# Performance work log

Measured on AMD Instinct MI355X. Metric: run time of the kernel, lower is better.

The kernel has to match this reference:

```python
import jax, jax.numpy as jnp
import numpy as np

N_NODES = 50000
IN_CH = 128
OUT_CH = 64
HEADS = 2
N_EDGES = 400000
NEG_SLOPE = 0.2  # PyG GATConv default


def _glorot(key, shape):
    fan_in, fan_out = shape[0], shape[-1]
    lim = jnp.sqrt(6.0 / (fan_in + fan_out))
    return jax.random.uniform(key, shape, jnp.float32, -lim, lim)


def setup_inputs() -> dict:
    key = jax.random.key(0)
    ks = jax.random.split(key, 12)
    hid = 2 * OUT_CH  # per-head channels of conv1
    inp = {
        "x": jax.random.normal(ks[0], (N_NODES, IN_CH), jnp.float32),
        "edge_index": jax.random.randint(ks[1], (2, N_EDGES), 0, N_NODES, jnp.int32),
        # conv1: in=IN_CH, out=hid per head, HEADS heads, concat
        "W1": _glorot(ks[2], (IN_CH, HEADS * hid)),
        "att_src1": _glorot(ks[3], (HEADS, hid)),
        "att_dst1": _glorot(ks[4], (HEADS, hid)),
        "b1": jnp.zeros((HEADS * hid,), jnp.float32),
        # conv_mu: in=hid*HEADS, out=OUT_CH, 1 head
        "W_mu": _glorot(ks[5], (hid * HEADS, OUT_CH)),
        "att_src_mu": _glorot(ks[6], (1, OUT_CH)),
        "att_dst_mu": _glorot(ks[7], (1, OUT_CH)),
        "b_mu": jnp.zeros((OUT_CH,), jnp.float32),
        # conv_logstd: same shapes as conv_mu
        "W_ls": _glorot(ks[8], (hid * HEADS, OUT_CH)),
        "att_src_ls": _glorot(ks[9], (1, OUT_CH)),
        "att_dst_ls": _glorot(ks[10], (1, OUT_CH)),
        "b_ls": jnp.zeros((OUT_CH,), jnp.float32),
    }
    return inp


def gat_conv(x, src, dst, W, att_src, att_dst, b, n_nodes):
    """PyG GATConv (add_self_loops handled by caller in src/dst)."""
    H, C = att_src.shape
    h = (x @ W).reshape(n_nodes, H, C)                       # [N,H,C]
    a_src = jnp.einsum('nhc,hc->nh', h, att_src)             # [N,H]
    a_dst = jnp.einsum('nhc,hc->nh', h, att_dst)
    e = jax.nn.leaky_relu(a_src[src] + a_dst[dst], NEG_SLOPE)  # [E,H]
    # scatter-softmax over incoming edges per destination node
    m = jax.ops.segment_max(e, dst, num_segments=n_nodes)
    e = jnp.exp(e - m[dst])
    denom = jax.ops.segment_sum(e, dst, num_segments=n_nodes)
    alpha = e / (denom[dst] + 1e-16)                          # [E,H]
    out = jax.ops.segment_sum(h[src] * alpha[:, :, None], dst,
                              num_segments=n_nodes)           # [N,H,C]
    return out.reshape(n_nodes, H * C) + b


def reference(x, edge_index, W1, att_src1, att_dst1, b1,
              W_mu, att_src_mu, att_dst_mu, b_mu,
              W_ls, att_src_ls, att_dst_ls, b_ls):
    n = x.shape[0]
    loop = jnp.arange(n, dtype=edge_index.dtype)
    src = jnp.concatenate([edge_index[0], loop])  # add self-loops (PyG default)
    dst = jnp.concatenate([edge_index[1], loop])
    h = jax.nn.elu(gat_conv(x, src, dst, W1, att_src1, att_dst1, b1, n))
    mu = gat_conv(h, src, dst, W_mu, att_src_mu, att_dst_mu, b_mu, n)
    logstd = gat_conv(h, src, dst, W_ls, att_src_ls, att_dst_ls, b_ls, n)
    return (mu, logstd)
```

## Files before the change

### kernel.cpp

```cpp
#include <hip/hip_runtime.h>
#include <math.h>

#define N_NODES 50000
#define N_EDGES 400000
#define PAD 64

typedef __attribute__((ext_vector_type(8))) short bf16x8;
typedef __attribute__((ext_vector_type(4))) float f32x4;

__device__ __forceinline__ float lrelu(float x){ return x > 0.f ? x : 0.2f*x; }
__device__ __forceinline__ float bf2f(unsigned short u){ return __uint_as_float(((unsigned int)u)<<16); }
__device__ __forceinline__ unsigned short f2bf(float f){
    unsigned int b = __float_as_uint(f);
    return (unsigned short)((b + 0x7FFFu + ((b>>16)&1u)) >> 16);
}
__device__ __forceinline__ float4 bf4(ushort4 u){
    return make_float4(bf2f(u.x), bf2f(u.y), bf2f(u.z), bf2f(u.w));
}
__device__ __forceinline__ float wexp(float e){ return __expf(fminf(e, 80.f)); }

__global__ __launch_bounds__(256) void prep_k(const float* __restrict__ x, unsigned short* __restrict__ xb,
        const float* __restrict__ W1, const float* __restrict__ Wmu, const float* __restrict__ Wls,
        unsigned short* __restrict__ W1T, unsigned short* __restrict__ WmlT,
        const int* __restrict__ src, const int* __restrict__ dst,
        int* __restrict__ counts, int* __restrict__ csr_src){
    int i = blockIdx.x*256 + threadIdx.x;
    if (i < (N_NODES*128)/4){
        float4 v = ((const float4*)x)[i];
        ((ushort4*)xb)[i] = make_ushort4(f2bf(v.x), f2bf(v.y), f2bf(v.z), f2bf(v.w));
    }
    if (i < 32768){
        int n = i >> 7, k = i & 127;
        W1T[i] = f2bf(W1[k*256 + n]);
        int n2 = i >> 8, k2 = i & 255;
        float v = (n2 < 64) ? Wmu[k2*64 + n2] : Wls[k2*64 + (n2-64)];
        WmlT[i] = f2bf(v);
    }
    if (i < N_EDGES){
        int d = dst[i];
        int pos = atomicAdd(&counts[d], 1);
        csr_src[d*PAD + pos] = src[i];
    }
}

template<int MODE>
__global__ __launch_bounds__(256) void mfma_gemm_k(const unsigned short* __restrict__ A,
        const unsigned short* __restrict__ BT, unsigned short* __restrict__ C,
        int M, int K, int ldc,
        const float* __restrict__ attS0, const float* __restrict__ attD0,
        const float* __restrict__ attS1, const float* __restrict__ attD1,
        float* __restrict__ outS, float* __restrict__ outD){
    __shared__ unsigned short As[128*40];
    __shared__ unsigned short Bs[128*40];
    int t = threadIdx.x;
    int lane = t & 63, wid = t >> 6;
    int wy = wid >> 1, wx = wid & 1;
    int quad = lane >> 4, l15 = lane & 15;
    int row0 = blockIdx.y * 128;
    int col0 = blockIdx.x * 128;

    f32x4 acc[4][4];
    #pragma unroll
    for (int i = 0; i < 4; i++)
        #pragma unroll
        for (int j = 0; j < 4; j++)
            acc[i][j] = (f32x4){0.f, 0.f, 0.f, 0.f};

    int r = t >> 2;
    int cofs = (t & 3) * 8;

    for (int k0 = 0; k0 < K; k0 += 32){
        int gr0 = min(row0 + r,      M-1);
        int gr1 = min(row0 + r + 64, M-1);
        float4 av0 = *(const float4*)(A  + (size_t)gr0*K + k0 + cofs);
        float4 av1 = *(const float4*)(A  + (size_t)gr1*K + k0 + cofs);
        float4 bv0 = *(const float4*)(BT + (size_t)(col0 + r)*K      + k0 + cofs);
        float4 bv1 = *(const float4*)(BT + (size_t)(col0 + r + 64)*K + k0 + cofs);
        __syncthreads();
        *(float4*)&As[r*40 + cofs]      = av0;
        *(float4*)&As[(r+64)*40 + cofs] = av1;
        *(float4*)&Bs[r*40 + cofs]      = bv0;
        *(float4*)&Bs[(r+64)*40 + cofs] = bv1;
        __syncthreads();

        bf16x8 af[4], bf[4];
        #pragma unroll
        for (int i = 0; i < 4; i++)
            af[i] = *(const bf16x8*)&As[(wy*64 + i*16 + l15)*40 + quad*8];
        #pragma unroll
        for (int j = 0; j < 4; j++)
            bf[j] = *(const bf16x8*)&Bs[(wx*64 + j*16 + l15)*40 + quad*8];
        #pragma unroll
        for (int i = 0; i < 4; i++)
            #pragma unroll
            for (int j = 0; j < 4; j++)
                acc[i][j] = __builtin_amdgcn_mfma_f32_16x16x32_bf16(af[i], bf[j], acc[i][j], 0, 0, 0);
    }

    int head = blockIdx.x;
    float aS[4], aD[4];
    #pragma unroll
    for (int j = 0; j < 4; j++){
        if (MODE == 1){
            int ch = wx*64 + j*16 + l15;
            aS[j] = attS0[head*128 + ch];
            aD[j] = attD0[head*128 + ch];
        } else {
            int c2 = j*16 + l15;
            aS[j] = wx ? attS1[c2] : attS0[c2];
            aD[j] = wx ? attD1[c2] : attD0[c2];
        }
    }

    #pragma unroll
    for (int i = 0; i < 4; i++){
        #pragma unroll
        for (int reg = 0; reg < 4; reg++){
            int rr = row0 + wy*64 + i*16 + quad*4 + reg;
            float sp = 0.f, dp = 0.f;
            #pragma unroll
            for (int j = 0; j < 4; j++){
                float v = acc[i][j][reg];
                int cc = col0 + wx*64 + j*16 + l15;
                if (rr < M) C[(size_t)rr*ldc + cc] = f2bf(v);
                sp = fmaf(v, aS[j], sp);
                dp = fmaf(v, aD[j], dp);
            }
            #pragma unroll
            for (int msk = 1; msk < 16; msk <<= 1){
                sp += __shfl_xor(sp, msk);
                dp += __shfl_xor(dp, msk);
            }
            if (l15 == 0 && rr < M){
                if (MODE == 1){
                    atomicAdd(&outS[rr*2 + head], sp);
                    atomicAdd(&outD[rr*2 + head], dp);
                } else {
                    outS[rr*2 + wx] = sp;
                    outD[rr*2 + wx] = dp;
                }
            }
        }
    }
}

__global__ __launch_bounds__(256) void agg1_k(const unsigned short* __restrict__ h1,
        const float* __restrict__ as, const float* __restrict__ ad,
        const int* __restrict__ counts, const int* __restrict__ csr_src,
        const float* __restrict__ b1, unsigned short* __restrict__ hout){
    int wave = threadIdx.x >> 6, lane = threadIdx.x & 63;
    int n = blockIdx.x*4 + wave;
    if (n >= N_NODES) return;
    int head = lane >> 5;
    const ushort4* h1v = (const ushort4*)h1;

    float adh = ad[n*2 + head];
    float ash = as[n*2 + head];

    float w = wexp(lrelu(ash + adh));
    float l = w;
    float4 r = bf4(h1v[(size_t)n*64 + lane]);
    float4 acc = make_float4(w*r.x, w*r.y, w*r.z, w*r.w);

    int deg = counts[n];
    int off = n*PAD;
    int dm1 = deg - 1;
    for (int k = 0; k < deg; k += 8){
        int sidx[8];
        #pragma unroll
        for (int u = 0; u < 8; u++) sidx[u] = csr_src[off + min(k+u, dm1)];
        float w8[8];
        #pragma unroll
        for (int u = 0; u < 8; u++){
            float av = as[sidx[u]*2 + head];
            w8[u] = (k+u <= dm1) ? wexp(lrelu(av + adh)) : 0.f;
        }
        #pragma unroll
        for (int u = 0; u < 8; u++){
            float4 ru = bf4(h1v[(size_t)sidx[u]*64 + lane]);
            float wu = w8[u];
            l += wu;
            acc.x = fmaf(wu, ru.x, acc.x);
            acc.y = fmaf(wu, ru.y, acc.y);
            acc.z = fmaf(wu, ru.z, acc.z);
            acc.w = fmaf(wu, ru.w, acc.w);
        }
    }

    float invl = 1.f / (l + 1e-16f);
    float4 b4 = *(const float4*)&b1[lane*4];
    float4 v;
    v.x = acc.x*invl + b4.x; v.y = acc.y*invl + b4.y;
    v.z = acc.z*invl + b4.z; v.w = acc.w*invl + b4.w;
    v.x = v.x > 0.f ? v.x : __expf(v.x) - 1.f;
    v.y = v.y > 0.f ? v.y : __expf(v.y) - 1.f;
    v.z = v.z > 0.f ? v.z : __expf(v.z) - 1.f;
    v.w = v.w > 0.f ? v.w : __expf(v.w) - 1.f;
    ((ushort4*)hout)[(size_t)n*64 + lane] = make_ushort4(f2bf(v.x), f2bf(v.y), f2bf(v.z), f2bf(v.w));
}

__global__ __launch_bounds__(256) void agg2_k(const unsigned short* __restrict__ hml,
        const float* __restrict__ as, const float* __restrict__ ad,
        const int* __restrict__ counts, const int* __restrict__ csr_src,
        const float* __restrict__ b_mu, const float* __restrict__ b_ls,
        float* __restrict__ out){
    int grp = threadIdx.x >> 5, lane = threadIdx.x & 31;
    int n = blockIdx.x*8 + grp;
    if (n >= N_NODES) return;
    int g = lane >> 4;
    const ushort4* hv = (const ushort4*)hml;

    float adh = ad[n*2 + g];
    float ash = as[n*2 + g];

    float w = wexp(lrelu(ash + adh));
    float l = w;
    float4 r = bf4(hv[(size_t)n*32 + lane]);
    float4 acc = make_float4(w*r.x, w*r.y, w*r.z, w*r.w);

    int deg = counts[n];
    int off = n*PAD;
    int dm1 = deg - 1;
    for (int k = 0; k < deg; k += 8){
        int sidx[8];
        #pragma unroll
        for (int u = 0; u < 8; u++) sidx[u] = csr_src[off + min(k+u, dm1)];
        float w8[8];
        #pragma unroll
        for (int u = 0; u < 8; u++){
            float av = as[sidx[u]*2 + g];
            w8[u] = (k+u <= dm1) ? wexp(lrelu(av + adh)) : 0.f;
        }
        #pragma unroll
        for (int u = 0; u < 8; u++){
            float4 ru = bf4(hv[(size_t)sidx[u]*32 + lane]);
            float wu = w8[u];
            l += wu;
            acc.x = fmaf(wu, ru.x, acc.x);
            acc.y = fmaf(wu, ru.y, acc.y);
            acc.z = fmaf(wu, ru.z, acc.z);
            acc.w = fmaf(wu, ru.w, acc.w);
        }
    }

    float invl = 1.f / (l + 1e-16f);
    int c = (lane & 15) * 4;
    const float* bb = g ? b_ls : b_mu;
    float4 b4 = *(const float4*)&bb[c];
    float4 v;
    v.x = acc.x*invl + b4.x; v.y = acc.y*invl + b4.y;
    v.z = acc.z*invl + b4.z; v.w = acc.w*invl + b4.w;
    float* base = g ? (out + (size_t)N_NODES*64) : out;
    *(float4*)&base[(size_t)n*64 + c] = v;
}

extern "C" void kernel_launch(void* const* d_in, const int* in_sizes, int n_in,
                              void* d_out, int out_size, void* d_ws, size_t ws_size,
                              hipStream_t stream) {
    const float* x           = (const float*)d_in[0];
    const int*   ei          = (const int*)d_in[1];
    const float* W1          = (const float*)d_in[2];
    const float* att_src1    = (const float*)d_in[3];
    const float* att_dst1    = (const float*)d_in[4];
    const float* b1          = (const float*)d_in[5];
    const float* W_mu        = (const float*)d_in[6];
    const float* att_src_mu  = (const float*)d_in[7];
    const float* att_dst_mu  = (const float*)d_in[8];
    const float* b_mu        = (const float*)d_in[9];
    const float* W_ls        = (const float*)d_in[10];
    const float* att_src_ls  = (const float*)d_in[11];
    const float* att_dst_ls  = (const float*)d_in[12];
    const float* b_ls        = (const float*)d_in[13];
    float* out = (float*)d_out;

    const int* srcp = ei;
    const int* dstp = ei + N_EDGES;

    unsigned short* xb   = (unsigned short*)d_ws;
    unsigned short* h1   = xb   + (size_t)N_NODES*128;
    unsigned short* hbuf = h1   + (size_t)N_NODES*256;
    unsigned short* hml  = hbuf + (size_t)N_NODES*256;
    unsigned short* W1T  = hml  + (size_t)N_NODES*128;
    unsigned short* WmlT = W1T  + 32768;
    int*   counts = (int*)(WmlT + 32768);
    float* as1    = (float*)(counts + N_NODES);
    float* ad1    = as1 + 2*N_NODES;
    float* as2    = ad1 + 2*N_NODES;
    float* ad2    = as2 + 2*N_NODES;
    int*   csr    = (int*)(ad2 + 2*N_NODES);

    hipMemsetAsync(counts, 0, N_NODES*sizeof(int) + 4*N_NODES*sizeof(float), stream);

    prep_k<<<(N_NODES*128/4 + 255)/256, 256, 0, stream>>>(x, xb, W1, W_mu, W_ls, W1T, WmlT,
                                                          srcp, dstp, counts, csr);

    mfma_gemm_k<1><<<dim3(2, 391), 256, 0, stream>>>(xb, W1T, h1, N_NODES, 128, 256,
                                                     att_src1, att_dst1, nullptr, nullptr, as1, ad1);
    agg1_k<<<(N_NODES + 3) / 4, 256, 0, stream>>>(h1, as1, ad1, counts, csr, b1, hbuf);

    mfma_gemm_k<2><<<dim3(1, 391), 256, 0, stream>>>(hbuf, WmlT, hml, N_NODES, 256, 128,
                                                     att_src_mu, att_dst_mu, att_src_ls, att_dst_ls, as2, ad2);
    agg2_k<<<(N_NODES + 7) / 8, 256, 0, stream>>>(hml, as2, ad2, counts, csr, b_mu, b_ls, out);
}
```

Before: 236.9 us.

## Precompute normalized attention weights and split aggregation across column slices

Adds a wnorm_k kernel that computes each node's normalized softmax weights over its padded CSR neighbours once per layer. Aggregation becomes agg1s/agg2s, where each block handles 8 nodes times one 32-column slice, with one scalar bf16 per lane instead of ushort4 vectors. The goal is to avoid recomputing exp and the softmax sum inside the gather loop and to spread the gather over more blocks. In exchange it adds two kernel launches, extra weight-array traffic, narrower uncoalesced scalar gathers, and repeated csr/weight reads for every column slice. When the workspace is small (PW=32), weights for neighbours beyond 32 are never written but are still read.

New measurement: 321.6 us. +35.7%, slower.

```diff
diff --git a/kernel.cpp b/kernel.cpp
--- a/kernel.cpp
+++ b/kernel.cpp
@@ -13,9 +13,6 @@
 __device__ __forceinline__ unsigned short f2bf(float f){
     unsigned int b = __float_as_uint(f);
     return (unsigned short)((b + 0x7FFFu + ((b>>16)&1u)) >> 16);
-}
-__device__ __forceinline__ float4 bf4(ushort4 u){
-    return make_float4(bf2f(u.x), bf2f(u.y), bf2f(u.z), bf2f(u.w));
 }
 __device__ __forceinline__ float wexp(float e){ return __expf(fminf(e, 80.f)); }
 
@@ -144,114 +141,139 @@
     }
 }
 
-__global__ __launch_bounds__(256) void agg1_k(const unsigned short* __restrict__ h1,
-        const float* __restrict__ as, const float* __restrict__ ad,
+__global__ __launch_bounds__(256) void wnorm_k(const float* __restrict__ as, const float* __restrict__ ad,
         const int* __restrict__ counts, const int* __restrict__ csr_src,
+        float* __restrict__ w0, float* __restrict__ w1, float* __restrict__ wselfv, int PW){
+    int t = threadIdx.x;
+    int n = blockIdx.x*8 + (t >> 5);
+    int lane = t & 31;
+    if (n >= N_NODES) return;
+    int deg = counts[n], off = n*PAD;
+    float2 aD = ((const float2*)ad)[n];
+    float2 aS = ((const float2*)as)[n];
+    float ws0 = wexp(lrelu(aS.x + aD.x));
+    float ws1 = wexp(lrelu(aS.y + aD.y));
+    float wa0 = 0.f, wa1 = 0.f, wb0 = 0.f, wb1 = 0.f;
+    if (lane < deg){
+        float2 a = ((const float2*)as)[csr_src[off + lane]];
+        wa0 = wexp(lrelu(a.x + aD.x));
+        wa1 = wexp(lrelu(a.y + aD.y));
+    }
+    if (lane + 32 < deg){
+        float2 a = ((const float2*)as)[csr_src[off + lane + 32]];
+        wb0 = wexp(lrelu(a.x + aD.x));
+        wb1 = wexp(lrelu(a.y + aD.y));
+    }
+    float t0 = wa0 + wb0, t1 = wa1 + wb1;
+    #pragma unroll
+    for (int m = 1; m < 32; m <<= 1){
+        t0 += __shfl_xor(t0, m, 32);
+        t1 += __shfl_xor(t1, m, 32);
+    }
+    float inv0 = 1.f / (ws0 + t0 + 1e-16f);
+    float inv1 = 1.f / (ws1 + t1 + 1e-16f);
+    int ow = n*PW;
+    if (lane < deg && lane < PW){
+        w0[ow + lane] = wa0*inv0;
+        w1[ow + lane] = wa1*inv1;
+    }
+    if (lane + 32 < deg && lane + 32 < PW){
+        w0[ow + lane + 32] = wb0*inv0;
+        w1[ow + lane + 32] = wb1*inv1;
+    }
+    if (lane == 0)
+        ((float2*)wselfv)[n] = make_float2(ws0*inv0, ws1*inv1);
+}
+
+__global__ __launch_bounds__(256) void agg1s_k(const unsigned short* __restrict__ h1,
+        const int* __restrict__ counts, const int* __restrict__ csr_src,
+        const float* __restrict__ w0p, const float* __restrict__ w1p,
+        const float* __restrict__ wselfv, int PW,
         const float* __restrict__ b1, unsigned short* __restrict__ hout){
-    int wave = threadIdx.x >> 6, lane = threadIdx.x & 63;
-    int n = blockIdx.x*4 + wave;
-    if (n >= N_NODES) return;
-    int head = lane >> 5;
-    const ushort4* h1v = (const ushort4*)h1;
-
-    float adh = ad[n*2 + head];
-    float ash = as[n*2 + head];
-
-    float w = wexp(lrelu(ash + adh));
-    float l = w;
-    float4 r = bf4(h1v[(size_t)n*64 + lane]);
-    float4 acc = make_float4(w*r.x, w*r.y, w*r.z, w*r.w);
+    int gid = blockIdx.x;
+    int s = gid & 7, nb = gid >> 3;
+    int t = threadIdx.x;
+    int n = nb*8 + (t >> 5);
+    int lane = t & 31;
+    int c = s*32 + lane;
+    int head = s >> 2;
+    const float* cw = head ? w1p : w0p;
+
+    float wself = wselfv[n*2 + head];
+    float acc = wself * bf2f(h1[n*256 + c]);
 
     int deg = counts[n];
-    int off = n*PAD;
+    int off = n*PAD, ow = n*PW;
     int dm1 = deg - 1;
-    for (int k = 0; k < deg; k += 8){
-        int sidx[8];
-        #pragma unroll
-        for (int u = 0; u < 8; u++) sidx[u] = csr_src[off + min(k+u, dm1)];
-        float w8[8];
-        #pragma unroll
-        for (int u = 0; u < 8; u++){
-            float av = as[sidx[u]*2 + head];
-            w8[u] = (k+u <= dm1) ? wexp(lrelu(av + adh)) : 0.f;
-        }
-        #pragma unroll
-        for (int u = 0; u < 8; u++){
-            float4 ru = bf4(h1v[(size_t)sidx[u]*64 + lane]);
-            float wu = w8[u];
-            l += wu;
-            acc.x = fmaf(wu, ru.x, acc.x);
-            acc.y = fmaf(wu, ru.y, acc.y);
-            acc.z = fmaf(wu, ru.z, acc.z);
-            acc.w = fmaf(wu, ru.w, acc.w);
-        }
-    }
-
-    float invl = 1.f / (l + 1e-16f);
-    float4 b4 = *(const float4*)&b1[lane*4];
-    float4 v;
-    v.x = acc.x*invl + b4.x; v.y = acc.y*invl + b4.y;
-    v.z = acc.z*invl + b4.z; v.w = acc.w*invl + b4.w;
-    v.x = v.x > 0.f ? v.x : __expf(v.x) - 1.f;
-    v.y = v.y > 0.f ? v.y : __expf(v.y) - 1.f;
-    v.z = v.z > 0.f ? v.z : __expf(v.z) - 1.f;
-    v.w = v.w > 0.f ? v.w : __expf(v.w) - 1.f;
-    ((ushort4*)hout)[(size_t)n*64 + lane] = make_ushort4(f2bf(v.x), f2bf(v.y), f2bf(v.z), f2bf(v.w));
-}
-
-__global__ __launch_bounds__(256) void agg2_k(const unsigned short* __restrict__ hml,
-        const float* __restrict__ as, const float* __restrict__ ad,
+    for (int k = 0; k < deg; k += 4){
+        int i0 = csr_src[off + k];
+        int i1 = csr_src[off + min(k+1, dm1)];
+        int i2 = csr_src[off + min(k+2, dm1)];
+        int i3 = csr_src[off + min(k+3, dm1)];
+        float u0 = cw[ow + k];
+        float u1 = (k+1 <= dm1) ? cw[ow + k+1] : 0.f;
+        float u2 = (k+2 <= dm1) ? cw[ow + k+2] : 0.f;
+        float u3 = (k+3 <= dm1) ? cw[ow + k+3] : 0.f;
+        float r0 = bf2f(h1[i0*256 + c]);
+        float r1 = bf2f(h1[i1*256 + c]);
+        float r2 = bf2f(h1[i2*256 + c]);
+        float r3 = bf2f(h1[i3*256 + c]);
+        acc = fmaf(u0, r0, acc);
+        acc = fmaf(u1, r1, acc);
+        acc = fmaf(u2, r2, acc);
+        acc = fmaf(u3, r3, acc);
+    }
+
+    float v = acc + b1[c];
+    v = v > 0.f ? v : __expf(v) - 1.f;
+    hout[n*256 + c] = f2bf(v);
+}
+
+__global__ __launch_bounds__(256) void agg2s_k(const unsigned short* __restrict__ hml,
         const int* __restrict__ counts, const int* __restrict__ csr_src,
+        const float* __restrict__ w0p, const float* __restrict__ w1p,
+        const float* __restrict__ wselfv, int PW,
         const float* __restrict__ b_mu, const float* __restrict__ b_ls,
         float* __restrict__ out){
-    int grp = threadIdx.x >> 5, lane = threadIdx.x & 31;
-    int n = blockIdx.x*8 + grp;
-    if (n >= N_NODES) return;
-    int g = lane >> 4;
-    const ushort4* hv = (const ushort4*)hml;
-
-    float adh = ad[n*2 + g];
-    float ash = as[n*2 + g];
-
-    float w = wexp(lrelu(ash + adh));
-    float l = w;
-    float4 r = bf4(hv[(size_t)n*32 + lane]);
-    float4 acc = make_float4(w*r.x, w*r.y, w*r.z, w*r.w);
+    int gid = blockIdx.x;
+    int s = gid & 7, nb = gid >> 3;
+    int cs = s & 3, nh = s >> 2;
+    int t = threadIdx.x;
+    int n = nh*25000 + nb*8 + (t >> 5);
+    int lane = t & 31;
+    int c = cs*32 + lane;
+    int g = cs >> 1;
+    const float* cw = g ? w1p : w0p;
+
+    float wself = wselfv[n*2 + g];
+    float acc = wself * bf2f(hml[n*128 + c]);
 
     int deg = counts[n];
-    int off = n*PAD;
+    int off = n*PAD, ow = n*PW;
     int dm1 = deg - 1;
-    for (int k = 0; k < deg; k += 8){
-        int sidx[8];
-        #pragma unroll
-        for (int u = 0; u < 8; u++) sidx[u] = csr_src[off + min(k+u, dm1)];
-        float w8[8];
-        #pragma unroll
-        for (int u = 0; u < 8; u++){
-            float av = as[sidx[u]*2 + g];
-            w8[u] = (k+u <= dm1) ? wexp(lrelu(av + adh)) : 0.f;
-        }
-        #pragma unroll
-        for (int u = 0; u < 8; u++){
-            float4 ru = bf4(hv[(size_t)sidx[u]*32 + lane]);
-            float wu = w8[u];
-            l += wu;
-            acc.x = fmaf(wu, ru.x, acc.x);
-            acc.y = fmaf(wu, ru.y, acc.y);
-            acc.z = fmaf(wu, ru.z, acc.z);
-            acc.w = fmaf(wu, ru.w, acc.w);
-        }
-    }
-
-    float invl = 1.f / (l + 1e-16f);
-    int c = (lane & 15) * 4;
+    for (int k = 0; k < deg; k += 4){
+        int i0 = csr_src[off + k];
+        int i1 = csr_src[off + min(k+1, dm1)];
+        int i2 = csr_src[off + min(k+2, dm1)];
+        int i3 = csr_src[off + min(k+3, dm1)];
+        float u0 = cw[ow + k];
+        float u1 = (k+1 <= dm1) ? cw[ow + k+1] : 0.f;
+        float u2 = (k+2 <= dm1) ? cw[ow + k+2] : 0.f;
+        float u3 = (k+3 <= dm1) ? cw[ow + k+3] : 0.f;
+        float r0 = bf2f(hml[i0*128 + c]);
+        float r1 = bf2f(hml[i1*128 + c]);
+        float r2 = bf2f(hml[i2*128 + c]);
+        float r3 = bf2f(hml[i3*128 + c]);
+        acc = fmaf(u0, r0, acc);
+        acc = fmaf(u1, r1, acc);
+        acc = fmaf(u2, r2, acc);
+        acc = fmaf(u3, r3, acc);
+    }
+
+    int col = c & 63;
     const float* bb = g ? b_ls : b_mu;
-    float4 b4 = *(const float4*)&bb[c];
-    float4 v;
-    v.x = acc.x*invl + b4.x; v.y = acc.y*invl + b4.y;
-    v.z = acc.z*invl + b4.z; v.w = acc.w*invl + b4.w;
     float* base = g ? (out + (size_t)N_NODES*64) : out;
-    *(float4*)&base[(size_t)n*64 + c] = v;
+    base[(size_t)n*64 + col] = acc + bb[col];
 }
 
 extern "C" void kernel_launch(void* const* d_in, const int* in_sizes, int n_in,
@@ -288,6 +310,26 @@
     float* as2    = ad1 + 2*N_NODES;
     float* ad2    = as2 + 2*N_NODES;
     int*   csr    = (int*)(ad2 + 2*N_NODES);
+    char*  tail   = (char*)(csr + (size_t)N_NODES*PAD);
+    size_t base_bytes = (size_t)(tail - (char*)d_ws);
+
+    int PW;
+    float *w0_1, *w1_1, *w0_2, *w1_2, *wself;
+    size_t need64 = base_bytes + (size_t)N_NODES*64*2*sizeof(float) + (size_t)N_NODES*2*sizeof(float);
+    if (ws_size >= need64){
+        PW = 64;
+        w0_1 = (float*)tail;
+        w1_1 = w0_1 + (size_t)N_NODES*64;
+        wself = w1_1 + (size_t)N_NODES*64;
+        w0_2 = w0_1; w1_2 = w1_1;
+    } else {
+        PW = 32;
+        w0_1 = (float*)xb;
+        w1_1 = w0_1 + (size_t)N_NODES*32;
+        w0_2 = (float*)h1;
+        w1_2 = w0_2 + (size_t)N_NODES*32;
+        wself = (float*)tail;
+    }
 
     hipMemsetAsync(counts, 0, N_NODES*sizeof(int) + 4*N_NODES*sizeof(float), stream);
 
@@ -296,9 +338,11 @@
 
     mfma_gemm_k<1><<<dim3(2, 391), 256, 0, stream>>>(xb, W1T, h1, N_NODES, 128, 256,
                                                      att_src1, att_dst1, nullptr, nullptr, as1, ad1);
-    agg1_k<<<(N_NODES + 3) / 4, 256, 0, stream>>>(h1, as1, ad1, counts, csr, b1, hbuf);
+    wnorm_k<<<(N_NODES + 7) / 8, 256, 0, stream>>>(as1, ad1, counts, csr, w0_1, w1_1, wself, PW);
+    agg1s_k<<<50000, 256, 0, stream>>>(h1, counts, csr, w0_1, w1_1, wself, PW, b1, hbuf);
 
     mfma_gemm_k<2><<<dim3(1, 391), 256, 0, stream>>>(hbuf, WmlT, hml, N_NODES, 256, 128,
                                                      att_src_mu, att_dst_mu, att_src_ls, att_dst_ls, as2, ad2);
-    agg2_k<<<(N_NODES + 7) / 8, 256, 0, stream>>>(hml, as2, ad2, counts, csr, b_mu, b_ls, out);
-}
+    wnorm_k<<<(N_NODES + 7) / 8, 256, 0, stream>>>(as2, ad2, counts, csr, w0_2, w1_2, wself, PW);
+    agg2s_k<<<25000, 256, 0, stream>>>(hml, counts, csr, w0_2, w1_2, wself, PW, b_mu, b_ls, out);
+}
```
